# Optimization experiments

Measured on AMD Instinct MI355X. Metric: run time of the kernel, lower is better.

The kernel has to match this reference:

```python
import jax, jax.numpy as jnp
import numpy as np

B, C_IN, H, W = 8, 112, 16, 16
D = 128            # patch_embed_dim
N_BANK = 200000
CHUNK = 1024       # query_chunk_size
NN_K = 3
TOPK_RATIO = 0.03  # reduction = 'topk_mean'


def setup_inputs() -> dict:
    key = jax.random.key(0)
    k1, k2, k3 = jax.random.split(key, 3)
    feature_map = jax.random.normal(k1, (B, C_IN, H, W), dtype=jnp.float32)
    proj_w = jax.random.normal(k2, (D, C_IN), dtype=jnp.float32) * 0.05
    memory_bank = jax.random.normal(k3, (N_BANK, D), dtype=jnp.float32)
    return {"feature_map": feature_map, "proj_w": proj_w, "memory_bank": memory_bank}


def _l2norm(x, axis=-1, eps=1e-12):
    return x / jnp.maximum(jnp.linalg.norm(x, axis=axis, keepdims=True), eps)


def reference(feature_map, proj_w, memory_bank):
    b, c, h, w = feature_map.shape
    patches = h * w
    # patch embeddings: NHWC flatten -> linear proj (no bias) -> L2 normalize
    emb = feature_map.transpose(0, 2, 3, 1).reshape(-1, c)        # [Q, C_in]
    emb = _l2norm(emb @ proj_w.T)                                  # [Q, D]
    bank = _l2norm(memory_bank)                                    # [N, D]
    bank_t = bank.T                                                # [D, N]

    q_total = emb.shape[0]
    n_chunks = q_total // CHUNK if q_total % CHUNK == 0 else -(-q_total // CHUNK)
    pad = n_chunks * CHUNK - q_total
    emb_p = jnp.pad(emb, ((0, pad), (0, 0)))
    chunks = emb_p.reshape(n_chunks, CHUNK, -1)

    def chunk_fn(q):                                               # q: [CHUNK, D]
        sims = q @ bank_t                                          # [CHUNK, N]
        best_sim, _ = jax.lax.top_k(sims, NN_K)                    # [CHUNK, k]
        dist = jnp.sqrt(jnp.maximum(2.0 - 2.0 * best_sim, 0.0))
        return dist.mean(axis=1)                                   # [CHUNK]

    patch_d = jax.lax.map(chunk_fn, chunks).reshape(-1)[:q_total]
    patch_d = patch_d.reshape(b, patches)                          # [B, P]

    # topk_mean reduction over patches
    k = min(patches, max(1, int(np.ceil(patches * TOPK_RATIO))))
    top_vals, _ = jax.lax.top_k(patch_d, k)
    return top_vals.mean(axis=1)                                   # [B]
```

## Files before the change

kernel.cpp:

```cpp
#include <hip/hip_runtime.h>
#include <stdint.h>

#define N_BANK 200000
#define N_PAD  201600
#define NQ     2048
#define DIMD   128
#define C_IN   112
#define NCHUNK 63
#define CHUNK_COLS 3200
#define NSTEP  25
#define NCE    126
#define NC3    378

typedef short v8s __attribute__((ext_vector_type(8)));
typedef float v4f __attribute__((ext_vector_type(4)));

typedef const __attribute__((address_space(1))) uint32_t* gp1_t;
typedef __attribute__((address_space(3))) uint32_t* lp3_t;

__device__ __forceinline__ void async16(const void* g, void* l) {
  __builtin_amdgcn_global_load_lds((gp1_t)g, (lp3_t)l, 16, 0, 0);
}

__device__ __forceinline__ unsigned short f2bf(float f) {
  uint32_t u = __float_as_uint(f);
  u += 0x7fff + ((u >> 16) & 1);
  return (unsigned short)(u >> 16);
}

__device__ __forceinline__ void insert3(float& m1, float& m2, float& m3, float v) {
  m3 = __builtin_amdgcn_fmed3f(m2, m3, v);
  m2 = __builtin_amdgcn_fmed3f(m1, m2, v);
  m1 = fmaxf(m1, v);
}

__global__ void emb_kernel(const float* __restrict__ fm, const float* __restrict__ pw,
                           unsigned short* __restrict__ embB) {
  int q = blockIdx.x;
  int b = q >> 8, p = q & 255;
  int tid = threadIdx.x;
  __shared__ float x[C_IN];
  __shared__ float wsum[2];
  if (tid < C_IN) x[tid] = fm[(b * C_IN + tid) * 256 + p];
  __syncthreads();
  const float* row = pw + tid * C_IN;
  float dot = 0.f;
#pragma unroll
  for (int c = 0; c < C_IN; ++c) dot = fmaf(x[c], row[c], dot);
  float s = dot * dot;
#pragma unroll
  for (int off = 32; off; off >>= 1) s += __shfl_xor(s, off);
  int lane = tid & 63, wv = tid >> 6;
  if (lane == 0) wsum[wv] = s;
  __syncthreads();
  float ss = wsum[0] + wsum[1];
  float scale = 1.f / fmaxf(sqrtf(ss), 1e-12f);
  int j = tid >> 3, pos = tid & 7;
  int sw = j ^ (q & 15);
  embB[q * DIMD + sw * 8 + pos] = f2bf(dot * scale);
}

__global__ void bank_kernel(const float* __restrict__ bank, unsigned short* __restrict__ bankB) {
  int tid = threadIdx.x;
  int wv = tid >> 6, lane = tid & 63;
  int r = blockIdx.x * 4 + wv;
  if (r >= N_PAD) return;
  uint32_t* out = (uint32_t*)bankB;
  int j = lane >> 2, w = lane & 3;
  int sdw = ((j ^ (r & 15)) << 2) | w;
  if (r < N_BANK) {
    float2 v = ((const float2*)bank)[r * 64 + lane];
    float s = v.x * v.x + v.y * v.y;
#pragma unroll
    for (int off = 32; off; off >>= 1) s += __shfl_xor(s, off);
    float scale = 1.f / fmaxf(sqrtf(s), 1e-12f);
    uint32_t lo = f2bf(v.x * scale);
    uint32_t hi = f2bf(v.y * scale);
    out[r * 64 + sdw] = lo | (hi << 16);
  } else {
    out[r * 64 + sdw] = 0u;
  }
}

__global__ __launch_bounds__(256, 2)
void sim_top3_kernel(const unsigned short* __restrict__ embB,
                     const unsigned short* __restrict__ bankB,
                     float* __restrict__ partial) {
  int mt = blockIdx.x;
  int chunk = blockIdx.y;
  int q0 = mt * 128;
  int tid = threadIdx.x;
  int wv = tid >> 6, lane = tid & 63;
  int wr = wv >> 1, wc = wv & 1;
  int g = lane >> 4, c0 = lane & 15;

  __shared__ __align__(16) unsigned char lds[32768];

  {
    const char* gbase = (const char*)embB + q0 * 256;
#pragma unroll
    for (int i = 0; i < 8; ++i) {
      int off = (wv * 8 + i) * 1024 + lane * 16;
      async16(gbase + off, lds + off);
    }
  }
  __syncthreads();

  v8s a[4][4];
#pragma unroll
  for (int fm = 0; fm < 4; ++fm)
#pragma unroll
    for (int k = 0; k < 4; ++k) {
      int row = wr * 64 + fm * 16 + c0;
      a[fm][k] = *(const v8s*)(lds + row * 256 + (((k * 4 + g) ^ c0) << 4));
    }

  float m1[16], m2[16], m3[16];
#pragma unroll
  for (int t = 0; t < 16; ++t) { m1[t] = -1e30f; m2[t] = -1e30f; m3[t] = -1e30f; }

  const char* bbase = (const char*)bankB + (size_t)chunk * CHUNK_COLS * 256;
  for (int s = 0; s < NSTEP; ++s) {
    __syncthreads();
#pragma unroll
    for (int i = 0; i < 8; ++i) {
      int off = (wv * 8 + i) * 1024 + lane * 16;
      async16(bbase + (size_t)s * 128 * 256 + off, lds + off);
    }
    __syncthreads();

#pragma unroll
    for (int fn = 0; fn < 4; ++fn) {
      v8s bf[4];
      int col = wc * 64 + fn * 16 + c0;
#pragma unroll
      for (int k = 0; k < 4; ++k)
        bf[k] = *(const v8s*)(lds + col * 256 + (((k * 4 + g) ^ c0) << 4));
#pragma unroll
      for (int fm = 0; fm < 4; ++fm) {
        v4f acc = {0.f, 0.f, 0.f, 0.f};
#pragma unroll
        for (int k = 0; k < 4; ++k)
          acc = __builtin_amdgcn_mfma_f32_16x16x32_bf16(a[fm][k], bf[k], acc, 0, 0, 0);
#pragma unroll
        for (int j = 0; j < 4; ++j)
          insert3(m1[fm * 4 + j], m2[fm * 4 + j], m3[fm * 4 + j], acc[j]);
      }
    }
  }

#pragma unroll
  for (int mask = 1; mask < 16; mask <<= 1) {
#pragma unroll
    for (int t = 0; t < 16; ++t) {
      float b1 = __shfl_xor(m1[t], mask);
      float b2 = __shfl_xor(m2[t], mask);
      float b3 = __shfl_xor(m3[t], mask);
      insert3(m1[t], m2[t], m3[t], b1);
      insert3(m1[t], m2[t], m3[t], b2);
      insert3(m1[t], m2[t], m3[t], b3);
    }
  }

  if (c0 == 0) {
    int ce = chunk * 2 + wc;
#pragma unroll
    for (int t = 0; t < 16; ++t) {
      int q = q0 + wr * 64 + (t >> 2) * 16 + g * 4 + (t & 3);
      float* dst = partial + (size_t)q * NC3 + ce * 3;
      dst[0] = m1[t];
      dst[1] = m2[t];
      dst[2] = m3[t];
    }
  }
}

__global__ void merge1_kernel(const float* __restrict__ partial, float* __restrict__ pd) {
  int q = (blockIdx.x * blockDim.x + threadIdx.x) >> 6;
  int lane = threadIdx.x & 63;
  const float* src = partial + (size_t)q * NC3;
  float m1 = -1e30f, m2 = -1e30f, m3 = -1e30f;
  for (int c = lane; c < NC3; c += 64) insert3(m1, m2, m3, src[c]);
#pragma unroll
  for (int mask = 32; mask; mask >>= 1) {
    float b1 = __shfl_xor(m1, mask);
    float b2 = __shfl_xor(m2, mask);
    float b3 = __shfl_xor(m3, mask);
    insert3(m1, m2, m3, b1);
    insert3(m1, m2, m3, b2);
    insert3(m1, m2, m3, b3);
  }
  if (lane == 0) {
    float d1 = sqrtf(fmaxf(2.f - 2.f * m1, 0.f));
    float d2 = sqrtf(fmaxf(2.f - 2.f * m2, 0.f));
    float d3 = sqrtf(fmaxf(2.f - 2.f * m3, 0.f));
    pd[q] = (d1 + d2 + d3) * (1.f / 3.f);
  }
}

__global__ void merge2_kernel(const float* __restrict__ pd, float* __restrict__ out) {
  int b = blockIdx.x;
  int tid = threadIdx.x;
  __shared__ float vals[256];
  __shared__ float rv[256];
  __shared__ int ri[256];
  vals[tid] = pd[b * 256 + tid];
  __syncthreads();
  float sum = 0.f;
  for (int iter = 0; iter < 8; ++iter) {
    rv[tid] = vals[tid]; ri[tid] = tid;
    __syncthreads();
    for (int s = 128; s > 0; s >>= 1) {
      if (tid < s && rv[tid + s] > rv[tid]) { rv[tid] = rv[tid + s]; ri[tid] = ri[tid + s]; }
      __syncthreads();
    }
    sum += rv[0];
    if (tid == 0) vals[ri[0]] = -1e30f;
    __syncthreads();
  }
  if (tid == 0) out[b] = sum * (1.f / 8.f);
}

extern "C" void kernel_launch(void* const* d_in, const int* in_sizes, int n_in,
                              void* d_out, int out_size, void* d_ws, size_t ws_size,
                              hipStream_t stream) {
  const float* fm   = (const float*)d_in[0];
  const float* pw   = (const float*)d_in[1];
  const float* bank = (const float*)d_in[2];
  float* out = (float*)d_out;

  char* ws = (char*)d_ws;
  unsigned short* bankB = (unsigned short*)ws;
  unsigned short* embB  = (unsigned short*)(ws + 51609600);
  float* partial        = (float*)(ws + 51609600 + 524288);
  float* pd             = (float*)(ws + 51609600 + 524288 + 3096576);

  emb_kernel<<<NQ, 128, 0, stream>>>(fm, pw, embB);
  bank_kernel<<<N_PAD / 4, 256, 0, stream>>>(bank, bankB);
  sim_top3_kernel<<<dim3(16, NCHUNK), 256, 0, stream>>>(embB, bankB, partial);
  merge1_kernel<<<NQ / 4, 256, 0, stream>>>(partial, pd);
  merge2_kernel<<<8, 256, 0, stream>>>(pd, out);
}
```

Measured before the change: 310.8 us.

## Double-buffer bank tiles in LDS and remap blocks for XCD-local chunk reuse

The similarity kernel now streams the bank in 64-column steps into two alternating 16KB LDS buffers. The next tile is prefetched asynchronously while MFMAs run on the current one, using explicit vmcnt waits and raw barriers in place of two __syncthreads per step. The grid is flattened and block IDs are remapped so the 16 query tiles sharing a bank chunk land on the same XCD (id&7), which improves L2 reuse of bank data. Each step does half the MFMA work, so there are twice as many barriers, and the hand-written waitcnt sequencing could race if it is miscounted.

After: 310.7 us. No clear change (-0.0%).

```diff
diff --git a/kernel.cpp b/kernel.cpp
--- a/kernel.cpp
+++ b/kernel.cpp
@@ -8,7 +8,8 @@
 #define C_IN   112
 #define NCHUNK 63
 #define CHUNK_COLS 3200
-#define NSTEP  25
+#define STEP_COLS 64
+#define NSTEP  50
 #define NCE    126
 #define NC3    378
 
@@ -86,8 +87,17 @@
 void sim_top3_kernel(const unsigned short* __restrict__ embB,
                      const unsigned short* __restrict__ bankB,
                      float* __restrict__ partial) {
-  int mt = blockIdx.x;
-  int chunk = blockIdx.y;
+  int id = blockIdx.x;
+  int chunk, mt;
+  if (id < 896) {
+    int x = id & 7, j = id >> 3;
+    chunk = x * 7 + (j >> 4);
+    mt = j & 15;
+  } else {
+    int t2 = id - 896;
+    chunk = 56 + (t2 >> 4);
+    mt = t2 & 15;
+  }
   int q0 = mt * 128;
   int tid = threadIdx.x;
   int wv = tid >> 6, lane = tid & 63;
@@ -100,11 +110,13 @@
     const char* gbase = (const char*)embB + q0 * 256;
 #pragma unroll
     for (int i = 0; i < 8; ++i) {
-      int off = (wv * 8 + i) * 1024 + lane * 16;
+      int off = i * 4096 + tid * 16;
       async16(gbase + off, lds + off);
     }
   }
-  __syncthreads();
+  asm volatile("s_waitcnt vmcnt(0)" ::: "memory");
+  __builtin_amdgcn_sched_barrier(0);
+  __builtin_amdgcn_s_barrier();
 
   v8s a[4][4];
 #pragma unroll
@@ -114,28 +126,46 @@
       int row = wr * 64 + fm * 16 + c0;
       a[fm][k] = *(const v8s*)(lds + row * 256 + (((k * 4 + g) ^ c0) << 4));
     }
+  asm volatile("s_waitcnt lgkmcnt(0)" ::: "memory");
+  __builtin_amdgcn_sched_barrier(0);
+  __builtin_amdgcn_s_barrier();
 
   float m1[16], m2[16], m3[16];
 #pragma unroll
   for (int t = 0; t < 16; ++t) { m1[t] = -1e30f; m2[t] = -1e30f; m3[t] = -1e30f; }
 
   const char* bbase = (const char*)bankB + (size_t)chunk * CHUNK_COLS * 256;
+
+#pragma unroll
+  for (int i = 0; i < 4; ++i) {
+    int off = i * 4096 + tid * 16;
+    async16(bbase + off, lds + off);
+  }
+
   for (int s = 0; s < NSTEP; ++s) {
-    __syncthreads();
-#pragma unroll
-    for (int i = 0; i < 8; ++i) {
-      int off = (wv * 8 + i) * 1024 + lane * 16;
-      async16(bbase + (size_t)s * 128 * 256 + off, lds + off);
-    }
-    __syncthreads();
-
-#pragma unroll
-    for (int fn = 0; fn < 4; ++fn) {
+    if (s + 1 < NSTEP) {
+      const char* gsrc = bbase + (size_t)(s + 1) * (STEP_COLS * 256);
+      unsigned char* ldst = lds + ((s + 1) & 1) * 16384;
+#pragma unroll
+      for (int i = 0; i < 4; ++i) {
+        int off = i * 4096 + tid * 16;
+        async16(gsrc + off, ldst + off);
+      }
+      asm volatile("s_waitcnt vmcnt(4)" ::: "memory");
+    } else {
+      asm volatile("s_waitcnt vmcnt(0)" ::: "memory");
+    }
+    __builtin_amdgcn_sched_barrier(0);
+    __builtin_amdgcn_s_barrier();
+
+    const unsigned char* bp = lds + (s & 1) * 16384;
+#pragma unroll
+    for (int fn = 0; fn < 2; ++fn) {
       v8s bf[4];
-      int col = wc * 64 + fn * 16 + c0;
+      int col = wc * 32 + fn * 16 + c0;
 #pragma unroll
       for (int k = 0; k < 4; ++k)
-        bf[k] = *(const v8s*)(lds + col * 256 + (((k * 4 + g) ^ c0) << 4));
+        bf[k] = *(const v8s*)(bp + col * 256 + (((k * 4 + g) ^ c0) << 4));
 #pragma unroll
       for (int fm = 0; fm < 4; ++fm) {
         v4f acc = {0.f, 0.f, 0.f, 0.f};
@@ -147,6 +177,7 @@
           insert3(m1[fm * 4 + j], m2[fm * 4 + j], m3[fm * 4 + j], acc[j]);
       }
     }
+    __builtin_amdgcn_s_barrier();
   }
 
 #pragma unroll
@@ -237,7 +268,7 @@
 
   emb_kernel<<<NQ, 128, 0, stream>>>(fm, pw, embB);
   bank_kernel<<<N_PAD / 4, 256, 0, stream>>>(bank, bankB);
-  sim_top3_kernel<<<dim3(16, NCHUNK), 256, 0, stream>>>(embB, bankB, partial);
+  sim_top3_kernel<<<16 * NCHUNK, 256, 0, stream>>>(embB, bankB, partial);
   merge1_kernel<<<NQ / 4, 256, 0, stream>>>(partial, pd);
   merge2_kernel<<<8, 256, 0, stream>>>(pd, out);
 }
```
